# Optimization experiments

Measured on AMD Instinct MI355X. Metric: run time of the kernel, lower is better.

The kernel has to match this reference:

```python
import jax, jax.numpy as jnp
from jax import lax
import numpy as np


def _conv2d(x, w, pad, dil=1):
    return lax.conv_general_dilated(x, w, (1, 1), [(pad, pad), (pad, pad)],
                                    rhs_dilation=(dil, dil),
                                    dimension_numbers=('NCHW', 'OIHW', 'NCHW'))


def _conv1d(x, w):
    # x [B,C,L], w [O,I,K], 'same' padding
    k = w.shape[2]
    return lax.conv_general_dilated(x, w, (1,), [(k // 2, k // 2)],
                                    dimension_numbers=('NCH', 'OIH', 'NCH'))


def _scan_fwd(slices, w):
    # slices [L,B,C,M]; s[i] += relu(conv1d(s[i-1])) for i=1..L-1 (sequential, carries updates)
    def f(c, r):
        n = r + jax.nn.relu(_conv1d(c, w))
        return n, n
    _, out = lax.scan(f, slices[0], slices[1:])
    return jnp.concatenate([slices[:1], out], axis=0)


def _scan_bwd(slices, w):
    # s[i] += relu(conv1d(s[i+1])) for i = L-2 .. 1 (first and last slice untouched)
    def f(c, r):
        n = r + jax.nn.relu(_conv1d(c, w))
        return n, n
    _, out = lax.scan(f, slices[-1], slices[-2:0:-1])
    return jnp.concatenate([slices[:1], out[::-1], slices[-1:]], axis=0)


def _resize_bilinear_ac(x, oh, ow):
    # bilinear, align_corners=True, x [B,C,H,W]
    H, W = x.shape[2], x.shape[3]
    ys = jnp.linspace(0.0, H - 1.0, oh)
    xs = jnp.linspace(0.0, W - 1.0, ow)
    y0 = jnp.floor(ys).astype(jnp.int32); y1 = jnp.minimum(y0 + 1, H - 1)
    x0 = jnp.floor(xs).astype(jnp.int32); x1 = jnp.minimum(x0 + 1, W - 1)
    wy = (ys - y0)[:, None]
    wx = xs - x0
    r = x[:, :, y0, :] * (1.0 - wy) + x[:, :, y1, :] * wy  # [B,C,oh,W]
    return r[:, :, :, x0] * (1.0 - wx) + r[:, :, :, x1] * wx


def reference(x, w11, s11, b11, w12, s12, b12, w21, s21, b21, w22, s22, b22,
              w31, s31, b31, w32, s32, b32, w33, s33, b33,
              w41, s41, b41, w42, s42, b42, w43, s43, b43,
              w51, s51, b51, w52, s52, b52, w53, s53, b53,
              w6, s6, b6, w7, s7, b7, wd, wu, wr, wl, w8, b8,
              fw9, fb9, fw10, fb10):
    def cbr(h, w, s, b, pad=1, dil=1):
        y = _conv2d(h, w, pad, dil)
        return jax.nn.relu(y * s[None, :, None, None] + b[None, :, None, None])

    def mp(h):
        B, C, H, W = h.shape
        return h.reshape(B, C, H // 2, 2, W // 2, 2).max((3, 5))

    x = cbr(x, w11, s11, b11); x = cbr(x, w12, s12, b12); x = mp(x)
    x = cbr(x, w21, s21, b21); x = cbr(x, w22, s22, b22); x = mp(x)
    x = cbr(x, w31, s31, b31); x = cbr(x, w32, s32, b32); x = cbr(x, w33, s33, b33); x = mp(x)
    x = cbr(x, w41, s41, b41); x = cbr(x, w42, s42, b42); x = cbr(x, w43, s43, b43)
    x = cbr(x, w51, s51, b51, pad=2, dil=2)
    x = cbr(x, w52, s52, b52, pad=2, dil=2)
    x = cbr(x, w53, s53, b53, pad=2, dil=2)
    x = cbr(x, w6, s6, b6, pad=4, dil=4)
    x = cbr(x, w7, s7, b7, pad=0)

    # SCNN spatial message passing (down, up over rows; right, left over cols)
    rows = jnp.moveaxis(x, 2, 0)            # [H,B,C,W]
    rows = _scan_fwd(rows, wd[:, :, 0, :])  # down
    rows = _scan_bwd(rows, wu[:, :, 0, :])  # up
    x = jnp.moveaxis(rows, 0, 2)
    cols = jnp.moveaxis(x, 3, 0)            # [W,B,C,H]
    cols = _scan_fwd(cols, wr[:, :, :, 0])  # right
    cols = _scan_bwd(cols, wl[:, :, :, 0])  # left
    x = jnp.moveaxis(cols, 0, 3)

    # dropout2d(p=0.1) treated as identity (deterministic/eval reference)
    x = _conv2d(x, w8, 0) + b8[None, :, None, None]  # [B,5,36,100]

    x1 = jax.nn.softmax(_resize_bilinear_ac(x, 288, 800), axis=1)

    x2 = jax.nn.softmax(x, axis=1)
    B, C, H, W = x2.shape
    x2 = x2.reshape(B, C, H // 2, 2, W // 2, 2).mean((3, 5)).reshape(B, -1)
    x2 = jax.nn.relu(x2 @ fw9.T + fb9)
    x2 = jax.nn.sigmoid(x2 @ fw10.T + fb10)
    return (x1, x2)


def setup_inputs():
    key = jax.random.key(0)
    ks = iter(jax.random.split(key, 80))

    def conv_w(ci, co, kh, kw):
        return jax.random.normal(next(ks), (co, ci, kh, kw), jnp.float32) * np.float32(np.sqrt(2.0 / (ci * kh * kw)))

    def bn(c):
        s = 0.9 + 0.2 * jax.random.uniform(next(ks), (c,), jnp.float32)
        b = 0.1 * jax.random.normal(next(ks), (c,), jnp.float32)
        return s, b

    d = {}
    d['x'] = jax.random.normal(next(ks), (4, 3, 288, 800), jnp.float32)
    specs = [('11', 3, 64), ('12', 64, 64), ('21', 64, 128), ('22', 128, 128),
             ('31', 128, 256), ('32', 256, 256), ('33', 256, 256),
             ('41', 256, 512), ('42', 512, 512), ('43', 512, 512),
             ('51', 512, 512), ('52', 512, 512), ('53', 512, 512)]
    for n, ci, co in specs:
        d['w' + n] = conv_w(ci, co, 3, 3)
        d['s' + n], d['b' + n] = bn(co)
    d['w6'] = conv_w(512, 1024, 3, 3); d['s6'], d['b6'] = bn(1024)
    d['w7'] = conv_w(1024, 128, 1, 1); d['s7'], d['b7'] = bn(128)
    # small scale keeps the 100-step additive recurrence numerically tame
    for n, (kh, kw) in (('wd', (1, 9)), ('wu', (1, 9)), ('wr', (9, 1)), ('wl', (9, 1))):
        d[n] = jax.random.normal(next(ks), (128, 128, kh, kw), jnp.float32) * 0.001
    d['w8'] = conv_w(128, 5, 1, 1)
    d['b8'] = 0.1 * jax.random.normal(next(ks), (5,), jnp.float32)
    d['fw9'] = jax.random.normal(next(ks), (128, 4500), jnp.float32) / np.float32(np.sqrt(4500.0))
    d['fb9'] = jnp.zeros((128,), jnp.float32)
    d['fw10'] = jax.random.normal(next(ks), (4, 128), jnp.float32) / np.float32(np.sqrt(128.0))
    d['fb10'] = jnp.zeros((4,), jnp.float32)
    return d
```

## Files before the change

kernel.cpp:

```cpp
#include <hip/hip_runtime.h>
#include <math.h>


#define NB 4

typedef unsigned short ushort_t;
typedef __attribute__((ext_vector_type(8))) short short8x;
typedef __attribute__((ext_vector_type(4))) float facc4;

static __device__ __forceinline__ ushort_t f2bh(float x) {
    unsigned u = __float_as_uint(x);
    unsigned r = u + 0x7fffu + ((u >> 16) & 1u);
    return (ushort_t)(r >> 16);
}
static __device__ __forceinline__ float bh2f(ushort_t h) {
    return __uint_as_float(((unsigned)h) << 16);
}
static __device__ __forceinline__ void split_store(float v, ushort_t* __restrict__ hi,
                                                   ushort_t* __restrict__ lo, size_t idx) {
    ushort_t h = f2bh(v);
    float l = v - bh2f(h);
    hi[idx] = h;
    lo[idx] = f2bh(l);
}
static __device__ __forceinline__ void ld8f(const float* p, float f[8]) {
    float4 a = *(const float4*)p;
    float4 b = *(const float4*)(p + 4);
    f[0] = a.x; f[1] = a.y; f[2] = a.z; f[3] = a.w;
    f[4] = b.x; f[5] = b.y; f[6] = b.z; f[7] = b.w;
}

__global__ __launch_bounds__(256) void repack_w_k(const float* __restrict__ w, float* __restrict__ wre,
                                                  int O, int IK) {
    int gid = blockIdx.x * 256 + threadIdx.x;
    if (gid >= O * IK) return;
    int o = gid / IK;
    int r = gid - o * IK;
    wre[r * O + o] = w[gid];
}

__global__ __launch_bounds__(256) void conv11_strip_k(const float* __restrict__ X0, const float* __restrict__ W11,
                                                      const float* __restrict__ sc, const float* __restrict__ bi,
                                                      ushort_t* __restrict__ Thi, ushort_t* __restrict__ Tlo, int r0) {
    int gid = blockIdx.x * 256 + threadIdx.x;
    if (gid >= 4 * 20 * 802 * 8) return;
    int c8 = gid & 7;
    int t = gid >> 3;
    int w = t % 802; t /= 802;
    int tr = t % 20;
    int b = t / 20;
    int gr = r0 - 1 + tr;
    int gc = w - 1;
    size_t obase = (((size_t)b * 20 + tr) * 802 + w) * 64 + c8 * 8;
    if (gr < 0 || gr >= 288 || gc < 0 || gc >= 800) {
#pragma unroll
        for (int j = 0; j < 8; ++j) { Thi[obase + j] = 0; Tlo[obase + j] = 0; }
        return;
    }
    float acc[8];
#pragma unroll
    for (int j = 0; j < 8; ++j) acc[j] = 0.f;
#pragma unroll
    for (int ci = 0; ci < 3; ++ci) {
        const float* inc = X0 + (size_t)(b * 3 + ci) * 288 * 800;
#pragma unroll
        for (int kh = 0; kh < 3; ++kh) {
            int ih = gr + kh - 1;
            if (ih < 0 || ih >= 288) continue;
#pragma unroll
            for (int kw = 0; kw < 3; ++kw) {
                int iw = gc + kw - 1;
                if (iw < 0 || iw >= 800) continue;
                float v = inc[ih * 800 + iw];
                float wf[8];
                ld8f(W11 + (ci * 9 + kh * 3 + kw) * 64 + c8 * 8, wf);
#pragma unroll
                for (int j = 0; j < 8; ++j) acc[j] = fmaf(v, wf[j], acc[j]);
            }
        }
    }
#pragma unroll
    for (int j = 0; j < 8; ++j) {
        int n = c8 * 8 + j;
        float r = acc[j] * sc[n] + bi[n];
        r = r > 0.f ? r : 0.f;
        split_store(r, Thi, Tlo, obase + j);
    }
}

__global__ __launch_bounds__(256) void repack_wmfma_k(const float* __restrict__ w, ushort_t* __restrict__ whi,
                                                      ushort_t* __restrict__ wlo, int N, int Cin, int taps) {
    int gid = blockIdx.x * 256 + threadIdx.x;
    if (gid >= N * Cin * taps) return;
    int o = gid / (Cin * taps);
    int r = gid - o * Cin * taps;
    int i = r / taps;
    int t = r - i * taps;
    float x = w[gid];
    size_t d = ((size_t)t * N + o) * Cin + i;
    ushort_t h = f2bh(x);
    whi[d] = h;
    wlo[d] = f2bh(x - bh2f(h));
}

__global__ __launch_bounds__(256) void vpool2_k(const ushort_t* __restrict__ shi, const ushort_t* __restrict__ slo,
                                                ushort_t* __restrict__ dhi, ushort_t* __restrict__ dlo,
                                                int Hs, int Wp, int C, int Hop, int Wop, int pad, int pr0) {
    int total = 4 * (Hs >> 1) * Wp * C;
    int gid = blockIdx.x * 256 + threadIdx.x;
    if (gid >= total) return;
    int c = gid % C;
    int t = gid / C;
    int w = t % Wp; t /= Wp;
    int hp = t % (Hs >> 1);
    int b = t / (Hs >> 1);
    size_t a0 = (((size_t)b * Hs + 2 * hp) * Wp + w) * C + c;
    size_t a1 = a0 + (size_t)Wp * C;
    float v0 = bh2f(shi[a0]) + bh2f(slo[a0]);
    float v1 = bh2f(shi[a1]) + bh2f(slo[a1]);
    float v = fmaxf(v0, v1);
    size_t d = (((size_t)b * Hop + pr0 + hp + pad) * Wop + (w + pad)) * C + c;
    split_store(v, dhi, dlo, d);
}

template <int MODE>
__global__ __launch_bounds__(256) void mfma_conv_k(
    const ushort_t* __restrict__ Ahi, const ushort_t* __restrict__ Alo,
    const ushort_t* __restrict__ Whi, const ushort_t* __restrict__ Wlo,
    const float* __restrict__ sc, const float* __restrict__ bi,
    ushort_t* __restrict__ Ohi, ushort_t* __restrict__ Olo, float* __restrict__ Fo,
    int M, int Wimg, int HS, int h0,
    int HpIn, int WpIn, int Cin, int ih0, int iph, int ipw, int dil, int taps,
    int N, int obst, int oh0, int oph, int opw, int WpOut) {
    __shared__ ushort_t sA0[128 * 40], sA1[128 * 40];
    __shared__ ushort_t sB0[64 * 40], sB1[64 * 40];

    int tid = threadIdx.x;
    int m0 = blockIdx.x * 128;
    int n0 = blockIdx.y * 64;

    int ar = tid >> 1;
    int ah = (tid & 1) * 16;
    int am = m0 + ar;
    if (am >= M) am = M - 1;
    int aw = am % Wimg;
    int t1 = am / Wimg;
    int ahh = h0 + t1 % HS;
    int ab = t1 / HS;

    int bp = tid >> 7;
    int bidx = tid & 127;
    int bn = bidx >> 1;
    int bh = (bidx & 1) * 16;
    const ushort_t* WP = bp ? Wlo : Whi;

    int wid = tid >> 6, lane = tid & 63;
    int moff = (wid >> 1) * 64, noff = (wid & 1) * 32;
    int lm = lane & 15, quad = lane >> 4;

    facc4 acc[4][2];
#pragma unroll
    for (int i = 0; i < 4; ++i)
#pragma unroll
        for (int j = 0; j < 2; ++j) acc[i][j] = (facc4)(0.f);

    for (int t = 0; t < taps; ++t) {
        int dh = 0, dw = 0;
        if (taps == 9) {
            dh = (t / 3 - 1) * dil;
            dw = (t % 3 - 1) * dil;
        }
        size_t aoff = (((size_t)ab * HpIn + (ahh - ih0 + iph + dh)) * WpIn + (aw + ipw + dw)) * Cin + ah;
        size_t boff0 = ((size_t)t * N + (n0 + bn)) * Cin + bh;
        for (int k0 = 0; k0 < Cin; k0 += 32) {
            {
                const ushort_t* p = Ahi + aoff + k0;
                uint4 v0 = *(const uint4*)p;
                uint4 v1 = *(const uint4*)(p + 8);
                *(uint4*)&sA0[ar * 40 + ah] = v0;
                *(uint4*)&sA0[ar * 40 + ah + 8] = v1;
                const ushort_t* q = Alo + aoff + k0;
                uint4 w0 = *(const uint4*)q;
                uint4 w1 = *(const uint4*)(q + 8);
                *(uint4*)&sA1[ar * 40 + ah] = w0;
                *(uint4*)&sA1[ar * 40 + ah + 8] = w1;
            }
            {
                const ushort_t* p = WP + boff0 + k0;
                uint4 v0 = *(const uint4*)p;
                uint4 v1 = *(const uint4*)(p + 8);
                ushort_t* dst = bp ? sB1 : sB0;
                *(uint4*)&dst[bn * 40 + bh] = v0;
                *(uint4*)&dst[bn * 40 + bh + 8] = v1;
            }
            __syncthreads();
            short8x afh[4], afl[4], bfh[2], bfl[2];
#pragma unroll
            for (int mi = 0; mi < 4; ++mi) {
                int base = (moff + mi * 16 + lm) * 40 + quad * 8;
                afh[mi] = *(const short8x*)&sA0[base];
                afl[mi] = *(const short8x*)&sA1[base];
            }
#pragma unroll
            for (int nj = 0; nj < 2; ++nj) {
                int base = (noff + nj * 16 + lm) * 40 + quad * 8;
                bfh[nj] = *(const short8x*)&sB0[base];
                bfl[nj] = *(const short8x*)&sB1[base];
            }
#pragma unroll
            for (int mi = 0; mi < 4; ++mi)
#pragma unroll
                for (int nj = 0; nj < 2; ++nj) {
                    acc[mi][nj] = __builtin_amdgcn_mfma_f32_16x16x32_bf16(afh[mi], bfh[nj], acc[mi][nj], 0, 0, 0);
                    acc[mi][nj] = __builtin_amdgcn_mfma_f32_16x16x32_bf16(afl[mi], bfh[nj], acc[mi][nj], 0, 0, 0);
                    acc[mi][nj] = __builtin_amdgcn_mfma_f32_16x16x32_bf16(afh[mi], bfl[nj], acc[mi][nj], 0, 0, 0);
                }
            __syncthreads();
        }
    }

#pragma unroll
    for (int mi = 0; mi < 4; ++mi)
#pragma unroll
        for (int nj = 0; nj < 2; ++nj) {
            int nglob = n0 + noff + nj * 16 + lm;
            float s = sc[nglob];
            float bb = bi[nglob];
            if (MODE == 1) {
#pragma unroll
                for (int rg = 0; rg < 4; rg += 2) {
                    int mg = m0 + moff + mi * 16 + quad * 4 + rg;
                    if (mg >= M) continue;
                    float v0 = acc[mi][nj][rg] * s + bb;
                    v0 = v0 > 0.f ? v0 : 0.f;
                    float v1 = acc[mi][nj][rg + 1] * s + bb;
                    v1 = v1 > 0.f ? v1 : 0.f;
                    float v = fmaxf(v0, v1);
                    int wq = mg % Wimg;
                    int tq = mg / Wimg;
                    int hq = h0 + tq % HS;
                    int bq = tq / HS;
                    size_t a = ((size_t)bq * obst + (size_t)(hq - oh0) * WpOut + (wq >> 1)) * N + nglob;
                    split_store(v, Ohi, Olo, a);
                }
            } else {
#pragma unroll
                for (int rg = 0; rg < 4; ++rg) {
                    int mg = m0 + moff + mi * 16 + quad * 4 + rg;
                    if (mg >= M) continue;
                    float v = acc[mi][nj][rg] * s + bb;
                    v = v > 0.f ? v : 0.f;
                    int wq = mg % Wimg;
                    int tq = mg / Wimg;
                    int hq = h0 + tq % HS;
                    int bq = tq / HS;
                    if (MODE == 0) {
                        size_t a = ((size_t)bq * obst + (size_t)(hq - oh0 + oph) * WpOut + (wq + opw)) * N + nglob;
                        split_store(v, Ohi, Olo, a);
                    } else {
                        size_t a = (((size_t)bq * N + nglob) * HS + (hq - h0)) * Wimg + wq;
                        Fo[a] = v;
                    }
                }
            }
        }
}

__global__ __launch_bounds__(256) void repack_scan_k(const float* __restrict__ w, float* __restrict__ wre) {
    int gid = blockIdx.x * 256 + threadIdx.x;
    if (gid >= 128 * 128 * 9) return;
    int o = gid / 1152;
    int r = gid - o * 1152;
    wre[r * 128 + o] = w[gid];
}

__global__ __launch_bounds__(256) void scan_row_k(float* __restrict__ F, const float* __restrict__ wsc, int hp, int hc) {
    __shared__ float sm[128 * 12];
    int b = blockIdx.x / 25;
    int w0 = (blockIdx.x % 25) * 4;
    int tid = threadIdx.x;
    const float* Fp = F + ((size_t)(b * 128) * 36 + hp) * 100;
    for (int i = tid; i < 1536; i += 256) {
        int ci = i / 12;
        int j = i - ci * 12;
        int iw = w0 - 4 + j;
        sm[i] = (iw >= 0 && iw < 100) ? Fp[(size_t)ci * 3600 + iw] : 0.f;
    }
    __syncthreads();
    int o = tid & 127;
    int half = tid >> 7;
    float a0 = 0.f, a1 = 0.f;
    for (int ci = 0; ci < 128; ++ci) {
        const float* s = sm + ci * 12 + half * 2;
        const float* wp = wsc + ci * 9 * 128 + o;
#pragma unroll
        for (int k = 0; k < 9; ++k) {
            float wt = wp[k * 128];
            a0 = fmaf(s[k], wt, a0);
            a1 = fmaf(s[k + 1], wt, a1);
        }
    }
    int w = w0 + half * 2;
    float* outp = F + ((size_t)(b * 128 + o) * 36 + hc) * 100 + w;
    outp[0] += a0 > 0.f ? a0 : 0.f;
    outp[1] += a1 > 0.f ? a1 : 0.f;
}

__global__ __launch_bounds__(256) void scan_col_k(float* __restrict__ F, const float* __restrict__ wsc, int wp_, int wc) {
    __shared__ float sm[128 * 12];
    int b = blockIdx.x / 9;
    int h0 = (blockIdx.x % 9) * 4;
    int tid = threadIdx.x;
    const float* Fp = F + (size_t)(b * 128 * 36) * 100 + wp_;
    for (int i = tid; i < 1536; i += 256) {
        int ci = i / 12;
        int j = i - ci * 12;
        int ih = h0 - 4 + j;
        sm[i] = (ih >= 0 && ih < 36) ? Fp[(size_t)(ci * 36 + ih) * 100] : 0.f;
    }
    __syncthreads();
    int o = tid & 127;
    int half = tid >> 7;
    float a0 = 0.f, a1 = 0.f;
    for (int ci = 0; ci < 128; ++ci) {
        const float* s = sm + ci * 12 + half * 2;
        const float* wp = wsc + ci * 9 * 128 + o;
#pragma unroll
        for (int k = 0; k < 9; ++k) {
            float wt = wp[k * 128];
            a0 = fmaf(s[k], wt, a0);
            a1 = fmaf(s[k + 1], wt, a1);
        }
    }
    int h = h0 + half * 2;
    float* outp = F + ((size_t)(b * 128 + o) * 36 + h) * 100 + wc;
    outp[0] += a0 > 0.f ? a0 : 0.f;
    outp[100] += a1 > 0.f ? a1 : 0.f;
}

__global__ __launch_bounds__(256) void conv8_k(const float* __restrict__ F, const float* __restrict__ w8,
                                               const float* __restrict__ b8, float* __restrict__ G) {
    int gid = blockIdx.x * 256 + threadIdx.x;
    if (gid >= NB * 3600) return;
    int hw = gid % 3600;
    int b = gid / 3600;
    float acc[5];
#pragma unroll
    for (int c = 0; c < 5; ++c) acc[c] = b8[c];
    const float* Fb = F + (size_t)b * 128 * 3600 + hw;
    for (int ci = 0; ci < 128; ++ci) {
        float v = Fb[(size_t)ci * 3600];
#pragma unroll
        for (int c = 0; c < 5; ++c) acc[c] = fmaf(v, w8[c * 128 + ci], acc[c]);
    }
#pragma unroll
    for (int c = 0; c < 5; ++c) G[(size_t)(b * 5 + c) * 3600 + hw] = acc[c];
}

__global__ __launch_bounds__(256) void resize_softmax_k(const float* __restrict__ G, float* __restrict__ out) {
    int gid = blockIdx.x * 256 + threadIdx.x;
    if (gid >= NB * 288 * 800) return;
    int ox = gid % 800;
    int t = gid / 800;
    int oy = t % 288;
    int b = t / 288;
    float fy = oy * (35.0f / 287.0f);
    int y0 = (int)fy; if (y0 > 34) y0 = 34;
    int y1 = y0 + 1;
    float wy = fy - y0;
    float fx = ox * (99.0f / 799.0f);
    int x0 = (int)fx; if (x0 > 98) x0 = 98;
    int x1 = x0 + 1;
    float wx = fx - x0;
    const float* Gb = G + (size_t)b * 5 * 3600;
    float v[5];
    float m = -1e30f;
#pragma unroll
    for (int c = 0; c < 5; ++c) {
        const float* Gc = Gb + (size_t)c * 3600;
        float a = Gc[y0 * 100 + x0] * (1.f - wx) + Gc[y0 * 100 + x1] * wx;
        float bb = Gc[y1 * 100 + x0] * (1.f - wx) + Gc[y1 * 100 + x1] * wx;
        v[c] = a * (1.f - wy) + bb * wy;
        m = fmaxf(m, v[c]);
    }
    float sum = 0.f;
#pragma unroll
    for (int c = 0; c < 5; ++c) { v[c] = expf(v[c] - m); sum += v[c]; }
    float inv = 1.f / sum;
#pragma unroll
    for (int c = 0; c < 5; ++c) out[((size_t)(b * 5 + c) * 288 + oy) * 800 + ox] = v[c] * inv;
}

__global__ __launch_bounds__(256) void pool_softmax_k(const float* __restrict__ G, float* __restrict__ P) {
    int gid = blockIdx.x * 256 + threadIdx.x;
    if (gid >= NB * 18 * 50) return;
    int pw = gid % 50;
    int t = gid / 50;
    int ph = t % 18;
    int b = t / 18;
    float s5[5] = {0.f, 0.f, 0.f, 0.f, 0.f};
    const float* Gb = G + (size_t)b * 5 * 3600;
#pragma unroll
    for (int dy = 0; dy < 2; ++dy) {
#pragma unroll
        for (int dx = 0; dx < 2; ++dx) {
            int hw = (2 * ph + dy) * 100 + (2 * pw + dx);
            float v[5], m = -1e30f, sum = 0.f;
#pragma unroll
            for (int c = 0; c < 5; ++c) { v[c] = Gb[(size_t)c * 3600 + hw]; m = fmaxf(m, v[c]); }
#pragma unroll
            for (int c = 0; c < 5; ++c) { v[c] = expf(v[c] - m); sum += v[c]; }
            float inv = 1.f / sum;
#pragma unroll
            for (int c = 0; c < 5; ++c) s5[c] += v[c] * inv;
        }
    }
#pragma unroll
    for (int c = 0; c < 5; ++c) P[b * 4500 + c * 900 + ph * 50 + pw] = s5[c] * 0.25f;
}

__global__ __launch_bounds__(256) void fc1_k(const float* __restrict__ P, const float* __restrict__ fw9,
                                             const float* __restrict__ fb9, float* __restrict__ H1) {
    int wid = blockIdx.x * 4 + (threadIdx.x >> 6);
    int lane = threadIdx.x & 63;
    if (wid >= 512) return;
    int b = wid >> 7;
    int o = wid & 127;
    const float* wr = fw9 + (size_t)o * 4500;
    const float* pr = P + b * 4500;
    float acc = 0.f;
    for (int i = lane; i < 4500; i += 64) acc = fmaf(wr[i], pr[i], acc);
    for (int s = 32; s > 0; s >>= 1) acc += __shfl_down(acc, s, 64);
    if (lane == 0) {
        float r = acc + fb9[o];
        H1[b * 128 + o] = r > 0.f ? r : 0.f;
    }
}

__global__ __launch_bounds__(64) void fc2_k(const float* __restrict__ H1, const float* __restrict__ fw10,
                                            const float* __restrict__ fb10, float* __restrict__ dout) {
    int t = threadIdx.x;
    if (t >= 16) return;
    int b = t >> 2;
    int o = t & 3;
    float acc = fb10[o];
    for (int i = 0; i < 128; ++i) acc = fmaf(H1[b * 128 + i], fw10[o * 128 + i], acc);
    dout[4608000 + t] = 1.f / (1.f + expf(-acc));
}

static inline int ceildiv(int a, int b) { return (a + b - 1) / b; }

extern "C" void kernel_launch(void* const* d_in, const int* in_sizes, int n_in,
                              void* d_out, int out_size, void* d_ws, size_t ws_size,
                              hipStream_t stream) {
    (void)in_sizes; (void)n_in; (void)out_size; (void)ws_size;
    char* U = (char*)d_ws;
    char* V = U + 19000064;

    float* W11f = (float*)(U);
    ushort_t* WM12 = (ushort_t*)(U + 8192);
    ushort_t* WM21 = (ushort_t*)(U + 155648);
    ushort_t* WM22 = (ushort_t*)(U + 450560);
    ushort_t* T1hi = (ushort_t*)(U + 1050624);
    ushort_t* T1lo = (ushort_t*)(U + 1050624 + 8212480);
    ushort_t* T3hi = (ushort_t*)(U + 1050624);
    ushort_t* T3lo = (ushort_t*)(U + 1050624 + 8232960);
    ushort_t* WMa = (ushort_t*)(U);
    ushort_t* WMb = (ushort_t*)(U + 4718592);
    float* WSC = (float*)(U);
    float* G = (float*)(U + 2359296);
    float* P = (float*)(U + 2647296);
    float* H1 = (float*)(U + 2719296);

    ushort_t* Xhi = (ushort_t*)(V);
    ushort_t* Xlo = (ushort_t*)(V + 15306752);
    ushort_t* S1hi = (ushort_t*)(V + 30613504);
    ushort_t* S1lo = (ushort_t*)(V + 60663808);
    ushort_t* T2hi = (ushort_t*)(V + 90714112);
    ushort_t* T2lo = (ushort_t*)(V + 90714112 + 3686400);
    ushort_t* Yhi = (ushort_t*)(V + 30613504);
    ushort_t* Ylo = (ushort_t*)(V + 61227008);
    ushort_t* Zhi = (ushort_t*)(V + 91840512);
    ushort_t* Zlo = (ushort_t*)(V + 97632256);
    ushort_t* HPhi = (ushort_t*)(V);
    ushort_t* HPlo = (ushort_t*)(V + 14745600);
    ushort_t* PAhi = (ushort_t*)(V + 30613504);
    ushort_t* PAlo = (ushort_t*)(V + 40345600);
    ushort_t* SBhi = (ushort_t*)(V + 50077696);
    ushort_t* SBlo = (ushort_t*)(V + 69541888);
    ushort_t* SAhi = (ushort_t*)(V);
    ushort_t* SAlo = (ushort_t*)(V + 19464192);
    ushort_t* C6hi = (ushort_t*)(V + 38928384);
    ushort_t* C6lo = (ushort_t*)(V + 68419584);
    float* F = (float*)(V);

    const float* X0 = (const float*)d_in[0];
    auto din = [&](int i) { return (const float*)d_in[i]; };
    auto wm_lo = [&](ushort_t* base, int taps, int N, int C) { return base + (size_t)taps * N * C; };

    repack_w_k<<<ceildiv(27 * 64, 256), 256, 0, stream>>>(din(1), W11f, 64, 27);
    repack_wmfma_k<<<ceildiv(64 * 64 * 9, 256), 256, 0, stream>>>(din(4), WM12, wm_lo(WM12, 9, 64, 64), 64, 64, 9);
    hipMemsetAsync(V + 30613504, 0, 60100608, stream);
    for (int s = 0; s < 16; ++s) {
        int r0 = s * 18;
        conv11_strip_k<<<2005, 256, 0, stream>>>(X0, W11f, din(2), din(3), T1hi, T1lo, r0);
        mfma_conv_k<1><<<dim3(450, 1), 256, 0, stream>>>(
            T1hi, T1lo, WM12, wm_lo(WM12, 9, 64, 64), din(5), din(6), T2hi, T2lo, nullptr,
            57600, 800, 18, r0, 20, 802, 64, r0, 1, 1, 1, 9, 64, 18 * 400, r0, 0, 0, 400);
        vpool2_k<<<ceildiv(4 * 9 * 400 * 64, 256), 256, 0, stream>>>(
            T2hi, T2lo, S1hi, S1lo, 18, 400, 64, 146, 402, 1, r0 / 2);
    }
    repack_wmfma_k<<<ceildiv(128 * 64 * 9, 256), 256, 0, stream>>>(din(7), WM21, wm_lo(WM21, 9, 128, 64), 128, 64, 9);
    repack_wmfma_k<<<ceildiv(128 * 128 * 9, 256), 256, 0, stream>>>(din(10), WM22, wm_lo(WM22, 9, 128, 128), 128, 128, 9);
    hipMemsetAsync(V, 0, 30613504, stream);
    for (int s = 0; s < 8; ++s) {
        int r0 = s * 18;
        int hstart = r0 - 1 < 0 ? 0 : r0 - 1;
        int hend = r0 + 19 > 144 ? 144 : r0 + 19;
        int rows = hend - hstart;
        int M21 = 4 * rows * 400;
        hipMemsetAsync(U + 1050624, 0, 16465920, stream);
        mfma_conv_k<0><<<dim3(ceildiv(M21, 128), 2), 256, 0, stream>>>(
            S1hi, S1lo, WM21, wm_lo(WM21, 9, 128, 64), din(8), din(9), T3hi, T3lo, nullptr,
            M21, 400, rows, hstart, 146, 402, 64, 0, 1, 1, 1, 9, 128, 20 * 402, r0 - 1, 0, 1, 402);
        mfma_conv_k<1><<<dim3(225, 2), 256, 0, stream>>>(
            T3hi, T3lo, WM22, wm_lo(WM22, 9, 128, 128), din(11), din(12), T2hi, T2lo, nullptr,
            28800, 400, 18, r0, 20, 402, 128, r0 - 1, 0, 1, 1, 9, 128, 18 * 200, r0, 0, 0, 200);
        vpool2_k<<<ceildiv(4 * 9 * 200 * 128, 256), 256, 0, stream>>>(
            T2hi, T2lo, Xhi, Xlo, 18, 200, 128, 74, 202, 1, r0 / 2);
    }

    repack_wmfma_k<<<ceildiv(256 * 128 * 9, 256), 256, 0, stream>>>(din(13), WMa, wm_lo(WMa, 9, 256, 128), 256, 128, 9);
    hipMemsetAsync(V + 30613504, 0, 61227008, stream);
    mfma_conv_k<0><<<dim3(450, 4), 256, 0, stream>>>(
        Xhi, Xlo, WMa, wm_lo(WMa, 9, 256, 128), din(14), din(15), Yhi, Ylo, nullptr,
        57600, 200, 72, 0, 74, 202, 128, 0, 1, 1, 1, 9, 256, 74 * 202, 0, 1, 1, 202);
    repack_wmfma_k<<<ceildiv(256 * 256 * 9, 256), 256, 0, stream>>>(din(16), WMa, wm_lo(WMa, 9, 256, 256), 256, 256, 9);
    repack_wmfma_k<<<ceildiv(256 * 256 * 9, 256), 256, 0, stream>>>(din(19), WMb, wm_lo(WMb, 9, 256, 256), 256, 256, 9);
    for (int s = 0; s < 6; ++s) {
        int h0s = s * 12;
        int hstart = h0s - 1 < 0 ? 0 : h0s - 1;
        int hend = h0s + 13 > 72 ? 72 : h0s + 13;
        int rows = hend - hstart;
        int M32 = 4 * rows * 200;
        hipMemsetAsync(V + 91840512, 0, 11583488, stream);
        mfma_conv_k<0><<<dim3(ceildiv(M32, 128), 4), 256, 0, stream>>>(
            Yhi, Ylo, WMa, wm_lo(WMa, 9, 256, 256), din(17), din(18), Zhi, Zlo, nullptr,
            M32, 200, rows, hstart, 74, 202, 256, 0, 1, 1, 1, 9, 256, 14 * 202, h0s - 1, 0, 1, 202);
        mfma_conv_k<1><<<dim3(75, 4), 256, 0, stream>>>(
            Zhi, Zlo, WMb, wm_lo(WMb, 9, 256, 256), din(20), din(21), HPhi, HPlo, nullptr,
            9600, 200, 12, h0s, 14, 202, 256, h0s - 1, 0, 1, 1, 9, 256, 72 * 100, 0, 0, 0, 100);
    }
    hipMemsetAsync(V + 30613504, 0, 19464192, stream);
    vpool2_k<<<ceildiv(4 * 36 * 100 * 256, 256), 256, 0, stream>>>(
        HPhi, HPlo, PAhi, PAlo, 72, 100, 256, 44, 108, 4, 0);

    struct L { int wi, si, bi, dil; };
    static const L l45[5] = {{25, 26, 27, 1}, {28, 29, 30, 1}, {31, 32, 33, 2}, {34, 35, 36, 2}, {37, 38, 39, 2}};
    repack_wmfma_k<<<ceildiv(512 * 256 * 9, 256), 256, 0, stream>>>(din(22), WMa, wm_lo(WMa, 9, 512, 256), 512, 256, 9);
    hipMemsetAsync(V + 50077696, 0, 38928384, stream);
    mfma_conv_k<0><<<dim3(113, 8), 256, 0, stream>>>(
        PAhi, PAlo, WMa, wm_lo(WMa, 9, 512, 256), din(23), din(24), SBhi, SBlo, nullptr,
        14400, 100, 36, 0, 44, 108, 256, 0, 4, 4, 1, 9, 512, 44 * 108, 0, 4, 4, 108);
    hipMemsetAsync(V, 0, 38928384, stream);
    for (int i = 0; i < 5; ++i) {
        const L& L0 = l45[i];
        repack_wmfma_k<<<ceildiv(512 * 512 * 9, 256), 256, 0, stream>>>(din(L0.wi), WMa, wm_lo(WMa, 9, 512, 512), 512, 512, 9);
        const ushort_t* ih = (i & 1) ? SAhi : SBhi;
        const ushort_t* il = (i & 1) ? SAlo : SBlo;
        ushort_t* oh = (i & 1) ? SBhi : SAhi;
        ushort_t* ol = (i & 1) ? SBlo : SAlo;
        mfma_conv_k<0><<<dim3(113, 8), 256, 0, stream>>>(
            ih, il, WMa, wm_lo(WMa, 9, 512, 512), din(L0.si), din(L0.bi), oh, ol, nullptr,
            14400, 100, 36, 0, 44, 108, 512, 0, 4, 4, L0.dil, 9, 512, 44 * 108, 0, 4, 4, 108);
    }
    repack_wmfma_k<<<ceildiv(1024 * 512 * 9, 256), 256, 0, stream>>>(din(40), WMa, wm_lo(WMa, 9, 1024, 512), 1024, 512, 9);
    mfma_conv_k<0><<<dim3(113, 16), 256, 0, stream>>>(
        SAhi, SAlo, WMa, wm_lo(WMa, 9, 1024, 512), din(41), din(42), C6hi, C6lo, nullptr,
        14400, 100, 36, 0, 44, 108, 512, 0, 4, 4, 4, 9, 1024, 3600, 0, 0, 0, 100);
    repack_wmfma_k<<<ceildiv(128 * 1024, 256), 256, 0, stream>>>(din(43), WMa, wm_lo(WMa, 1, 128, 1024), 128, 1024, 1);
    mfma_conv_k<2><<<dim3(113, 2), 256, 0, stream>>>(
        C6hi, C6lo, WMa, wm_lo(WMa, 1, 128, 1024), din(44), din(45), nullptr, nullptr, F,
        14400, 100, 36, 0, 36, 100, 1024, 0, 0, 0, 1, 1, 128, 0, 0, 0, 0, 0);

    for (int j = 0; j < 4; ++j)
        repack_scan_k<<<576, 256, 0, stream>>>(din(46 + j), WSC + (size_t)j * 147456);
    for (int h = 1; h <= 35; ++h)
        scan_row_k<<<100, 256, 0, stream>>>(F, WSC + 0 * 147456, h - 1, h);
    for (int h = 34; h >= 1; --h)
        scan_row_k<<<100, 256, 0, stream>>>(F, WSC + 1 * 147456, h + 1, h);
    for (int w = 1; w <= 99; ++w)
        scan_col_k<<<36, 256, 0, stream>>>(F, WSC + 2 * (size_t)147456, w - 1, w);
    for (int w = 98; w >= 1; --w)
        scan_col_k<<<36, 256, 0, stream>>>(F, WSC + 3 * (size_t)147456, w + 1, w);

    conv8_k<<<ceildiv(NB * 3600, 256), 256, 0, stream>>>(F, din(50), din(51), G);
    resize_softmax_k<<<ceildiv(NB * 288 * 800, 256), 256, 0, stream>>>(G, (float*)d_out);
    pool_softmax_k<<<ceildiv(NB * 18 * 50, 256), 256, 0, stream>>>(G, P);
    fc1_k<<<128, 256, 0, stream>>>(P, din(52), din(53), H1);
    fc2_k<<<1, 64, 0, stream>>>(H1, din(54), din(55), (float*)d_out);
}
```

Measured before the change: 12.09 ms.

## Widen MFMA conv N-tile to 128 and transpose feature map for column scans

```diff
diff --git a/kernel.cpp b/kernel.cpp
--- a/kernel.cpp
+++ b/kernel.cpp
@@ -123,7 +123,7 @@
     split_store(v, dhi, dlo, d);
 }
 
-template <int MODE>
+template <int MODE, int NJ>
 __global__ __launch_bounds__(256) void mfma_conv_k(
     const ushort_t* __restrict__ Ahi, const ushort_t* __restrict__ Alo,
     const ushort_t* __restrict__ Whi, const ushort_t* __restrict__ Wlo,
@@ -132,12 +132,13 @@
     int M, int Wimg, int HS, int h0,
     int HpIn, int WpIn, int Cin, int ih0, int iph, int ipw, int dil, int taps,
     int N, int obst, int oh0, int oph, int opw, int WpOut) {
+    constexpr int NT = NJ * 32;
     __shared__ ushort_t sA0[128 * 40], sA1[128 * 40];
-    __shared__ ushort_t sB0[64 * 40], sB1[64 * 40];
+    __shared__ ushort_t sB0[NT * 40], sB1[NT * 40];
 
     int tid = threadIdx.x;
     int m0 = blockIdx.x * 128;
-    int n0 = blockIdx.y * 64;
+    int n0 = blockIdx.y * NT;
 
     int ar = tid >> 1;
     int ah = (tid & 1) * 16;
@@ -148,21 +149,25 @@
     int ahh = h0 + t1 % HS;
     int ab = t1 / HS;
 
-    int bp = tid >> 7;
-    int bidx = tid & 127;
-    int bn = bidx >> 1;
-    int bh = (bidx & 1) * 16;
-    const ushort_t* WP = bp ? Wlo : Whi;
+    int br, bhh, bpl;
+    if (NJ == 4) {
+        br = tid >> 1; bhh = (tid & 1) * 16; bpl = 2;
+    } else {
+        int bp = tid >> 7;
+        int bidx = tid & 127;
+        br = bidx >> 1; bhh = (bidx & 1) * 16; bpl = bp;
+    }
 
     int wid = tid >> 6, lane = tid & 63;
-    int moff = (wid >> 1) * 64, noff = (wid & 1) * 32;
+    int moff = (wid >> 1) * 64;
+    int noff = (wid & 1) * (NJ * 16);
     int lm = lane & 15, quad = lane >> 4;
 
-    facc4 acc[4][2];
+    facc4 acc[4][NJ];
 #pragma unroll
     for (int i = 0; i < 4; ++i)
 #pragma unroll
-        for (int j = 0; j < 2; ++j) acc[i][j] = (facc4)(0.f);
+        for (int j = 0; j < NJ; ++j) acc[i][j] = (facc4)(0.f);
 
     for (int t = 0; t < taps; ++t) {
         int dh = 0, dw = 0;
@@ -171,7 +176,7 @@
             dw = (t % 3 - 1) * dil;
         }
         size_t aoff = (((size_t)ab * HpIn + (ahh - ih0 + iph + dh)) * WpIn + (aw + ipw + dw)) * Cin + ah;
-        size_t boff0 = ((size_t)t * N + (n0 + bn)) * Cin + bh;
+        size_t boff0 = ((size_t)t * N + (n0 + br)) * Cin + bhh;
         for (int k0 = 0; k0 < Cin; k0 += 32) {
             {
                 const ushort_t* p = Ahi + aoff + k0;
@@ -185,16 +190,27 @@
                 *(uint4*)&sA1[ar * 40 + ah] = w0;
                 *(uint4*)&sA1[ar * 40 + ah + 8] = w1;
             }
-            {
-                const ushort_t* p = WP + boff0 + k0;
+            if (NJ == 4) {
+                const ushort_t* p = Whi + boff0 + k0;
                 uint4 v0 = *(const uint4*)p;
                 uint4 v1 = *(const uint4*)(p + 8);
-                ushort_t* dst = bp ? sB1 : sB0;
-                *(uint4*)&dst[bn * 40 + bh] = v0;
-                *(uint4*)&dst[bn * 40 + bh + 8] = v1;
+                *(uint4*)&sB0[br * 40 + bhh] = v0;
+                *(uint4*)&sB0[br * 40 + bhh + 8] = v1;
+                const ushort_t* q = Wlo + boff0 + k0;
+                uint4 w0 = *(const uint4*)q;
+                uint4 w1 = *(const uint4*)(q + 8);
+                *(uint4*)&sB1[br * 40 + bhh] = w0;
+                *(uint4*)&sB1[br * 40 + bhh + 8] = w1;
+            } else {
+                const ushort_t* p = (bpl ? Wlo : Whi) + boff0 + k0;
+                uint4 v0 = *(const uint4*)p;
+                uint4 v1 = *(const uint4*)(p + 8);
+                ushort_t* dst = bpl ? sB1 : sB0;
+                *(uint4*)&dst[br * 40 + bhh] = v0;
+                *(uint4*)&dst[br * 40 + bhh + 8] = v1;
             }
             __syncthreads();
-            short8x afh[4], afl[4], bfh[2], bfl[2];
+            short8x afh[4], afl[4], bfh[NJ], bfl[NJ];
 #pragma unroll
             for (int mi = 0; mi < 4; ++mi) {
                 int base = (moff + mi * 16 + lm) * 40 + quad * 8;
@@ -202,7 +218,7 @@
                 afl[mi] = *(const short8x*)&sA1[base];
             }
 #pragma unroll
-            for (int nj = 0; nj < 2; ++nj) {
+            for (int nj = 0; nj < NJ; ++nj) {
                 int base = (noff + nj * 16 + lm) * 40 + quad * 8;
                 bfh[nj] = *(const short8x*)&sB0[base];
                 bfl[nj] = *(const short8x*)&sB1[base];
@@ -210,7 +226,7 @@
 #pragma unroll
             for (int mi = 0; mi < 4; ++mi)
 #pragma unroll
-                for (int nj = 0; nj < 2; ++nj) {
+                for (int nj = 0; nj < NJ; ++nj) {
                     acc[mi][nj] = __builtin_amdgcn_mfma_f32_16x16x32_bf16(afh[mi], bfh[nj], acc[mi][nj], 0, 0, 0);
                     acc[mi][nj] = __builtin_amdgcn_mfma_f32_16x16x32_bf16(afl[mi], bfh[nj], acc[mi][nj], 0, 0, 0);
                     acc[mi][nj] = __builtin_amdgcn_mfma_f32_16x16x32_bf16(afh[mi], bfl[nj], acc[mi][nj], 0, 0, 0);
@@ -222,7 +238,7 @@
 #pragma unroll
     for (int mi = 0; mi < 4; ++mi)
 #pragma unroll
-        for (int nj = 0; nj < 2; ++nj) {
+        for (int nj = 0; nj < NJ; ++nj) {
             int nglob = n0 + noff + nj * 16 + lm;
             float s = sc[nglob];
             float bb = bi[nglob];
@@ -306,17 +322,17 @@
     outp[1] += a1 > 0.f ? a1 : 0.f;
 }
 
-__global__ __launch_bounds__(256) void scan_col_k(float* __restrict__ F, const float* __restrict__ wsc, int wp_, int wc) {
+__global__ __launch_bounds__(256) void scan_colT_k(float* __restrict__ FT, const float* __restrict__ wsc, int wp_, int wc) {
     __shared__ float sm[128 * 12];
     int b = blockIdx.x / 9;
     int h0 = (blockIdx.x % 9) * 4;
     int tid = threadIdx.x;
-    const float* Fp = F + (size_t)(b * 128 * 36) * 100 + wp_;
+    const float* Fp = FT + (size_t)(b * 128) * 3600 + (size_t)wp_ * 36;
     for (int i = tid; i < 1536; i += 256) {
         int ci = i / 12;
         int j = i - ci * 12;
         int ih = h0 - 4 + j;
-        sm[i] = (ih >= 0 && ih < 36) ? Fp[(size_t)(ci * 36 + ih) * 100] : 0.f;
+        sm[i] = (ih >= 0 && ih < 36) ? Fp[(size_t)ci * 3600 + ih] : 0.f;
     }
     __syncthreads();
     int o = tid & 127;
@@ -333,9 +349,28 @@
         }
     }
     int h = h0 + half * 2;
-    float* outp = F + ((size_t)(b * 128 + o) * 36 + h) * 100 + wc;
+    float* outp = FT + ((size_t)(b * 128 + o) * 100 + wc) * 36 + h;
     outp[0] += a0 > 0.f ? a0 : 0.f;
-    outp[100] += a1 > 0.f ? a1 : 0.f;
+    outp[1] += a1 > 0.f ? a1 : 0.f;
+}
+
+__global__ __launch_bounds__(256) void transpose_fwd_k(const float* __restrict__ F, float* __restrict__ FT) {
+    int gid = blockIdx.x * 256 + threadIdx.x;
+    if (gid >= 4 * 128 * 3600) return;
+    int h = gid % 36;
+    int t = gid / 36;
+    int w = t % 100;
+    int bc = t / 100;
+    FT[gid] = F[(size_t)bc * 3600 + h * 100 + w];
+}
+__global__ __launch_bounds__(256) void transpose_bwd_k(const float* __restrict__ FT, float* __restrict__ F) {
+    int gid = blockIdx.x * 256 + threadIdx.x;
+    if (gid >= 4 * 128 * 3600) return;
+    int w = gid % 100;
+    int t = gid / 100;
+    int h = t % 36;
+    int bc = t / 36;
+    F[gid] = FT[(size_t)bc * 3600 + w * 36 + h];
 }
 
 __global__ __launch_bounds__(256) void conv8_k(const float* __restrict__ F, const float* __restrict__ w8,
@@ -493,6 +528,7 @@
     ushort_t* C6hi = (ushort_t*)(V + 38928384);
     ushort_t* C6lo = (ushort_t*)(V + 68419584);
     float* F = (float*)(V);
+    float* FT = (float*)(V + 7372800);
 
     const float* X0 = (const float*)d_in[0];
     auto din = [&](int i) { return (const float*)d_in[i]; };
@@ -504,7 +540,7 @@
     for (int s = 0; s < 16; ++s) {
         int r0 = s * 18;
         conv11_strip_k<<<2005, 256, 0, stream>>>(X0, W11f, din(2), din(3), T1hi, T1lo, r0);
-        mfma_conv_k<1><<<dim3(450, 1), 256, 0, stream>>>(
+        mfma_conv_k<1, 2><<<dim3(450, 1), 256, 0, stream>>>(
             T1hi, T1lo, WM12, wm_lo(WM12, 9, 64, 64), din(5), din(6), T2hi, T2lo, nullptr,
             57600, 800, 18, r0, 20, 802, 64, r0, 1, 1, 1, 9, 64, 18 * 400, r0, 0, 0, 400);
         vpool2_k<<<ceildiv(4 * 9 * 400 * 64, 256), 256, 0, stream>>>(
@@ -520,10 +556,10 @@
         int rows = hend - hstart;
         int M21 = 4 * rows * 400;
         hipMemsetAsync(U + 1050624, 0, 16465920, stream);
-        mfma_conv_k<0><<<dim3(ceildiv(M21, 128), 2), 256, 0, stream>>>(
+        mfma_conv_k<0, 4><<<dim3(ceildiv(M21, 128), 1), 256, 0, stream>>>(
             S1hi, S1lo, WM21, wm_lo(WM21, 9, 128, 64), din(8), din(9), T3hi, T3lo, nullptr,
             M21, 400, rows, hstart, 146, 402, 64, 0, 1, 1, 1, 9, 128, 20 * 402, r0 - 1, 0, 1, 402);
-        mfma_conv_k<1><<<dim3(225, 2), 256, 0, stream>>>(
+        mfma_conv_k<1, 4><<<dim3(225, 1), 256, 0, stream>>>(
             T3hi, T3lo, WM22, wm_lo(WM22, 9, 128, 128), din(11), din(12), T2hi, T2lo, nullptr,
             28800, 400, 18, r0, 20, 402, 128, r0 - 1, 0, 1, 1, 9, 128, 18 * 200, r0, 0, 0, 200);
         vpool2_k<<<ceildiv(4 * 9 * 200 * 128, 256), 256, 0, stream>>>(
@@ -532,7 +568,7 @@
 
     repack_wmfma_k<<<ceildiv(256 * 128 * 9, 256), 256, 0, stream>>>(din(13), WMa, wm_lo(WMa, 9, 256, 128), 256, 128, 9);
     hipMemsetAsync(V + 30613504, 0, 61227008, stream);
-    mfma_conv_k<0><<<dim3(450, 4), 256, 0, stream>>>(
+    mfma_conv_k<0, 4><<<dim3(450, 2), 256, 0, stream>>>(
         Xhi, Xlo, WMa, wm_lo(WMa, 9, 256, 128), din(14), din(15), Yhi, Ylo, nullptr,
         57600, 200, 72, 0, 74, 202, 128, 0, 1, 1, 1, 9, 256, 74 * 202, 0, 1, 1, 202);
     repack_wmfma_k<<<ceildiv(256 * 256 * 9, 256), 256, 0, stream>>>(din(16), WMa, wm_lo(WMa, 9, 256, 256), 256, 256, 9);
@@ -544,10 +580,10 @@
         int rows = hend - hstart;
         int M32 = 4 * rows * 200;
         hipMemsetAsync(V + 91840512, 0, 11583488, stream);
-        mfma_conv_k<0><<<dim3(ceildiv(M32, 128), 4), 256, 0, stream>>>(
+        mfma_conv_k<0, 4><<<dim3(ceildiv(M32, 128), 2), 256, 0, stream>>>(
             Yhi, Ylo, WMa, wm_lo(WMa, 9, 256, 256), din(17), din(18), Zhi, Zlo, nullptr,
             M32, 200, rows, hstart, 74, 202, 256, 0, 1, 1, 1, 9, 256, 14 * 202, h0s - 1, 0, 1, 202);
-        mfma_conv_k<1><<<dim3(75, 4), 256, 0, stream>>>(
+        mfma_conv_k<1, 4><<<dim3(75, 2), 256, 0, stream>>>(
             Zhi, Zlo, WMb, wm_lo(WMb, 9, 256, 256), din(20), din(21), HPhi, HPlo, nullptr,
             9600, 200, 12, h0s, 14, 202, 256, h0s - 1, 0, 1, 1, 9, 256, 72 * 100, 0, 0, 0, 100);
     }
@@ -559,7 +595,7 @@
     static const L l45[5] = {{25, 26, 27, 1}, {28, 29, 30, 1}, {31, 32, 33, 2}, {34, 35, 36, 2}, {37, 38, 39, 2}};
     repack_wmfma_k<<<ceildiv(512 * 256 * 9, 256), 256, 0, stream>>>(din(22), WMa, wm_lo(WMa, 9, 512, 256), 512, 256, 9);
     hipMemsetAsync(V + 50077696, 0, 38928384, stream);
-    mfma_conv_k<0><<<dim3(113, 8), 256, 0, stream>>>(
+    mfma_conv_k<0, 4><<<dim3(113, 4), 256, 0, stream>>>(
         PAhi, PAlo, WMa, wm_lo(WMa, 9, 512, 256), din(23), din(24), SBhi, SBlo, nullptr,
         14400, 100, 36, 0, 44, 108, 256, 0, 4, 4, 1, 9, 512, 44 * 108, 0, 4, 4, 108);
     hipMemsetAsync(V, 0, 38928384, stream);
@@ -570,16 +606,16 @@
         const ushort_t* il = (i & 1) ? SAlo : SBlo;
         ushort_t* oh = (i & 1) ? SBhi : SAhi;
         ushort_t* ol = (i & 1) ? SBlo : SAlo;
-        mfma_conv_k<0><<<dim3(113, 8), 256, 0, stream>>>(
+        mfma_conv_k<0, 4><<<dim3(113, 4), 256, 0, stream>>>(
             ih, il, WMa, wm_lo(WMa, 9, 512, 512), din(L0.si), din(L0.bi), oh, ol, nullptr,
             14400, 100, 36, 0, 44, 108, 512, 0, 4, 4, L0.dil, 9, 512, 44 * 108, 0, 4, 4, 108);
     }
     repack_wmfma_k<<<ceildiv(1024 * 512 * 9, 256), 256, 0, stream>>>(din(40), WMa, wm_lo(WMa, 9, 1024, 512), 1024, 512, 9);
-    mfma_conv_k<0><<<dim3(113, 16), 256, 0, stream>>>(
+    mfma_conv_k<0, 4><<<dim3(113, 8), 256, 0, stream>>>(
         SAhi, SAlo, WMa, wm_lo(WMa, 9, 1024, 512), din(41), din(42), C6hi, C6lo, nullptr,
         14400, 100, 36, 0, 44, 108, 512, 0, 4, 4, 4, 9, 1024, 3600, 0, 0, 0, 100);
     repack_wmfma_k<<<ceildiv(128 * 1024, 256), 256, 0, stream>>>(din(43), WMa, wm_lo(WMa, 1, 128, 1024), 128, 1024, 1);
-    mfma_conv_k<2><<<dim3(113, 2), 256, 0, stream>>>(
+    mfma_conv_k<2, 4><<<dim3(113, 1), 256, 0, stream>>>(
         C6hi, C6lo, WMa, wm_lo(WMa, 1, 128, 1024), din(44), din(45), nullptr, nullptr, F,
         14400, 100, 36, 0, 36, 100, 1024, 0, 0, 0, 1, 1, 128, 0, 0, 0, 0, 0);
 
@@ -589,10 +625,12 @@
         scan_row_k<<<100, 256, 0, stream>>>(F, WSC + 0 * 147456, h - 1, h);
     for (int h = 34; h >= 1; --h)
         scan_row_k<<<100, 256, 0, stream>>>(F, WSC + 1 * 147456, h + 1, h);
+    transpose_fwd_k<<<7200, 256, 0, stream>>>(F, FT);
     for (int w = 1; w <= 99; ++w)
-        scan_col_k<<<36, 256, 0, stream>>>(F, WSC + 2 * (size_t)147456, w - 1, w);
+        scan_colT_k<<<36, 256, 0, stream>>>(FT, WSC + 2 * (size_t)147456, w - 1, w);
     for (int w = 98; w >= 1; --w)
-        scan_col_k<<<36, 256, 0, stream>>>(F, WSC + 3 * (size_t)147456, w + 1, w);
+        scan_colT_k<<<36, 256, 0, stream>>>(FT, WSC + 3 * (size_t)147456, w + 1, w);
+    transpose_bwd_k<<<7200, 256, 0, stream>>>(FT, F);
 
     conv8_k<<<ceildiv(NB * 3600, 256), 256, 0, stream>>>(F, din(50), din(51), G);
     resize_softmax_k<<<ceildiv(NB * 288 * 800, 256), 256, 0, stream>>>(G, (float*)d_out);
```

Result: faster. 11.05 ms (-8.6%).
